# Kernel tuning notes

Measured on AMD Instinct MI355X. Metric: run time of the kernel, lower is better.

The kernel has to match this reference:

```python
import jax, jax.numpy as jnp
import numpy as np

N, D, V = 4096, 2048, 65536
IGNORE_INDEX = -100


def setup_inputs() -> dict:
    key = jax.random.key(0)
    k1, k2, k3 = jax.random.split(key, 3)
    e = jax.random.normal(k1, (N, D), dtype=jnp.float32)
    c = jax.random.normal(k2, (V, D), dtype=jnp.float32) * (D ** -0.5)
    targets = jax.random.randint(k3, (N,), 0, V, dtype=jnp.int64)
    # sprinkle some ignore_index entries to exercise masking
    targets = jnp.where(jnp.arange(N) % 97 == 0, IGNORE_INDEX, targets)
    return {"e": e, "c": c, "targets": targets}


def reference(e, c, targets):
    # logits = e @ c^T  -> [N, V] (the big intermediate CCE avoids materializing)
    logits = jnp.einsum("nd,vd->nv", e, c)
    lse = jax.nn.logsumexp(logits, axis=-1)  # [N]
    valid = targets != IGNORE_INDEX
    safe_t = jnp.where(valid, targets, 0)
    tgt_logit = jnp.take_along_axis(logits, safe_t[:, None], axis=-1)[:, 0]
    nll = jnp.where(valid, lse - tgt_logit, 0.0)
    count = jnp.maximum(jnp.sum(valid), 1)
    return jnp.sum(nll) / count.astype(nll.dtype)
```

## Files before the change

### kernel.cpp

```cpp
#include <hip/hip_runtime.h>
#include <hip/hip_bf16.h>
#include <hip/hip_fp8.h>

typedef __bf16 bf16_t;
typedef bf16_t bf16x8 __attribute__((ext_vector_type(8)));
typedef float f32x4 __attribute__((ext_vector_type(4)));
typedef float f32x16 __attribute__((ext_vector_type(16)));
typedef int   i32x4  __attribute__((ext_vector_type(4)));
typedef int   i32x8  __attribute__((ext_vector_type(8)));

#define N_ROWS 4096
#define DIM    2048
#define VOCAB  65536
#define IGN    (-100)

#define BM 128
#define BN 128
#define BK 128
#define NT (DIM / BK)
#define NUNITS (4 * NT)
#define SCALE1 0x7F7F7F7F

#define GLOAD_LDS16(gp, lp)                                                  \
  __builtin_amdgcn_global_load_lds(                                          \
      (const __attribute__((address_space(1))) void*)(gp),                   \
      (__attribute__((address_space(3))) void*)(lp), 16, 0, 0)

__global__ __launch_bounds__(256)
void cvt_fp8(const float* __restrict__ src, unsigned char* __restrict__ dst,
             long n16, float scale) {
  long i = (long)blockIdx.x * 256 + threadIdx.x;
  long stride = (long)gridDim.x * 256;
  for (; i < n16; i += stride) {
    const float4* s = reinterpret_cast<const float4*>(src) + i * 4;
    union { unsigned char b[16]; i32x4 v; } o;
#pragma unroll
    for (int q = 0; q < 4; ++q) {
      float4 a = s[q];
      o.b[q * 4 + 0] = __hip_fp8_e4m3(a.x * scale).__x;
      o.b[q * 4 + 1] = __hip_fp8_e4m3(a.y * scale).__x;
      o.b[q * 4 + 2] = __hip_fp8_e4m3(a.z * scale).__x;
      o.b[q * 4 + 3] = __hip_fp8_e4m3(a.w * scale).__x;
    }
    *reinterpret_cast<i32x4*>(dst + i * 16) = o.v;
  }
}

__global__ __launch_bounds__(256, 2)
void lce_gemm_fp8(const unsigned char* __restrict__ E8,
                  const unsigned char* __restrict__ C8,
                  float* __restrict__ sumexp) {
  extern __shared__ unsigned char lds[];
  const int tid = threadIdx.x;
  const int lane = tid & 63, wid = tid >> 6;
  const int wr = wid >> 1, wc = wid & 1;
  const int l31 = lane & 31, lh = lane >> 5;

  const int bid = blockIdx.x;
  const int wg = (bid & 7) * 2048 + (bid >> 3);
  const int brow = (wg & 31) * BM;
  const int bcol = (wg >> 5) * BN;

  const int g0 = wid * 64 + lane;
  const int g1 = 256 + g0;
  const int prel0 = g0 * 16;
  const int prel1 = g1 * 16;
  auto mkgoff = [&](int g) {
    int w = g >> 6, i = g & 63;
    return (size_t)(w * 16 + (i >> 2)) * DIM +
           (size_t)((((i & 3) ^ ((i >> 3) & 3)) << 4));
  };
  const size_t goff0 = mkgoff(g0), goff1 = mkgoff(g1);

  const unsigned char* Ebase = E8 + (size_t)brow * DIM;
  const unsigned char* Cbase = C8 + (size_t)bcol * DIM;

  auto stage = [&](int ug) {
    const unsigned char* gb = ((ug & 1) ? Cbase : Ebase) +
                              (ug >> 2) * BK + ((ug >> 1) & 1) * 64;
    unsigned char* lb = lds + (ug & 7) * 8192;
    GLOAD_LDS16(gb + goff0, lb + prel0);
    GLOAD_LDS16(gb + goff1, lb + prel1);
  };

  const int sw = (l31 >> 1) & 3;
  auto read_frag = [&](const unsigned char* U, int s) -> i32x8 {
    const unsigned char* p =
        U + s * 2048 + (l31 >> 4) * 1024 + (l31 & 15) * 64;
    i32x4 lo = *reinterpret_cast<const i32x4*>(p + (((lh * 2)     ^ sw) << 4));
    i32x4 hi = *reinterpret_cast<const i32x4*>(p + (((lh * 2 + 1) ^ sw) << 4));
    return __builtin_shufflevector(lo, hi, 0, 1, 2, 3, 4, 5, 6, 7);
  };

  f32x16 acc[2][2];
#pragma unroll
  for (int mi = 0; mi < 2; ++mi)
#pragma unroll
    for (int ni = 0; ni < 2; ++ni)
#pragma unroll
      for (int r = 0; r < 16; ++r) acc[mi][ni][r] = 0.f;

  stage(0); stage(1); stage(2); stage(3); stage(4); stage(5);
  asm volatile("s_waitcnt vmcnt(4)" ::: "memory");
  __builtin_amdgcn_s_barrier();

  i32x8 af0[2], bf0[2], af1[2], bf1[2];

  for (int T = 0; T < NT; ++T) {
    const unsigned char* base = lds + (T & 1) * 32768;
    const unsigned char* aU0 = base;
    const unsigned char* bU0 = base + 8192;
    const unsigned char* aU1 = base + 16384;
    const unsigned char* bU1 = base + 24576;

#pragma unroll
    for (int ni = 0; ni < 2; ++ni) bf0[ni] = read_frag(bU0, wc * 2 + ni);
#pragma unroll
    for (int mi = 0; mi < 2; ++mi) af0[mi] = read_frag(aU0, wr * 2 + mi);
    __builtin_amdgcn_sched_barrier(0);
#pragma unroll
    for (int ni = 0; ni < 2; ++ni) bf1[ni] = read_frag(bU1, wc * 2 + ni);
#pragma unroll
    for (int mi = 0; mi < 2; ++mi) af1[mi] = read_frag(aU1, wr * 2 + mi);
    __builtin_amdgcn_sched_barrier(0);

    stage(4 * T + 6);
    stage(4 * T + 7);
    asm volatile("s_waitcnt lgkmcnt(8)" ::: "memory");
    __builtin_amdgcn_sched_barrier(0);
    __builtin_amdgcn_s_setprio(1);
#pragma unroll
    for (int mi = 0; mi < 2; ++mi)
#pragma unroll
      for (int ni = 0; ni < 2; ++ni)
        acc[mi][ni] = __builtin_amdgcn_mfma_scale_f32_32x32x64_f8f6f4(
            af0[mi], bf0[ni], acc[mi][ni],
            0, 0, 0, SCALE1, 0, SCALE1);
    __builtin_amdgcn_s_setprio(0);
    __builtin_amdgcn_s_barrier();

    {
      const int ug = 4 * T + 8;
      if (ug < NUNITS) stage(ug);
      if (ug + 1 < NUNITS) stage(ug + 1);
    }
    asm volatile("s_waitcnt lgkmcnt(0)" ::: "memory");
    __builtin_amdgcn_sched_barrier(0);
    __builtin_amdgcn_s_setprio(1);
#pragma unroll
    for (int mi = 0; mi < 2; ++mi)
#pragma unroll
      for (int ni = 0; ni < 2; ++ni)
        acc[mi][ni] = __builtin_amdgcn_mfma_scale_f32_32x32x64_f8f6f4(
            af1[mi], bf1[ni], acc[mi][ni],
            0, 0, 0, SCALE1, 0, SCALE1);
    __builtin_amdgcn_s_setprio(0);
    if (T < NT - 1) {
      if (T < NT - 2) asm volatile("s_waitcnt vmcnt(4)" ::: "memory");
      else            asm volatile("s_waitcnt vmcnt(0)" ::: "memory");
    }
    __builtin_amdgcn_s_barrier();
  }

#pragma unroll
  for (int mi = 0; mi < 2; ++mi) {
    float p[16];
#pragma unroll
    for (int r = 0; r < 16; ++r)
      p[r] = __expf(acc[mi][0][r] * 0.125f) + __expf(acc[mi][1][r] * 0.125f);
#pragma unroll
    for (int m = 1; m < 32; m <<= 1)
#pragma unroll
      for (int r = 0; r < 16; ++r) p[r] += __shfl_xor(p[r], m, 64);
    if (l31 == 0) {
#pragma unroll
      for (int r = 0; r < 16; ++r) {
        const int row = brow + wr * 64 + mi * 32 + (r & 3) + 8 * (r >> 2) + 4 * lh;
        atomicAdd(&sumexp[row], p[r]);
      }
    }
  }
}

#define FBM 128
#define FBN 128
#define FBK 64
#define FNK (DIM / FBK)
#define FTHREADS 512

__global__ __launch_bounds__(FTHREADS, 4)
void lce_gemm_f32(const float* __restrict__ E, const float* __restrict__ C,
                  float* __restrict__ sumexp) {
  extern __shared__ unsigned char lds[];
  const int tid  = threadIdx.x;
  const int brow = blockIdx.x * FBM;
  const int bcol = blockIdx.y * FBN;

  float4 ra[4], rb[4];
  auto ld = [&](int k0) {
#pragma unroll
    for (int i = 0; i < 4; ++i) {
      int f = tid + i * FTHREADS;
      int r = f >> 4;
      int c = (f & 15) << 2;
      ra[i] = *reinterpret_cast<const float4*>(&E[(size_t)(brow + r) * DIM + k0 + c]);
      rb[i] = *reinterpret_cast<const float4*>(&C[(size_t)(bcol + r) * DIM + k0 + c]);
    }
  };
  auto st = [&](int buf) {
    unsigned char* a = lds + buf * 32768;
    unsigned char* b = a + 16384;
#pragma unroll
    for (int i = 0; i < 4; ++i) {
      int f  = tid + i * FTHREADS;
      int r  = f >> 4;
      int cbb = (f & 15) << 3;
      int off = r * 128 + (cbb ^ ((r & 7) << 4));
      union { bf16_t h[4]; unsigned long long u; } pa, pb;
      pa.h[0] = (bf16_t)ra[i].x; pa.h[1] = (bf16_t)ra[i].y;
      pa.h[2] = (bf16_t)ra[i].z; pa.h[3] = (bf16_t)ra[i].w;
      pb.h[0] = (bf16_t)rb[i].x; pb.h[1] = (bf16_t)rb[i].y;
      pb.h[2] = (bf16_t)rb[i].z; pb.h[3] = (bf16_t)rb[i].w;
      *reinterpret_cast<unsigned long long*>(a + off) = pa.u;
      *reinterpret_cast<unsigned long long*>(b + off) = pb.u;
    }
  };

  f32x4 acc[4][2];
#pragma unroll
  for (int mi = 0; mi < 4; ++mi)
#pragma unroll
    for (int ni = 0; ni < 2; ++ni) acc[mi][ni] = (f32x4){0.f, 0.f, 0.f, 0.f};

  const int lane = tid & 63, wid = tid >> 6;
  const int wr = wid >> 2, wc = wid & 3;
  const int l15 = lane & 15, lg = lane >> 4;
  const int swz = (l15 & 7) << 4;

  auto comp = [&](int buf) {
    const unsigned char* a = lds + buf * 32768;
    const unsigned char* b = a + 16384;
#pragma unroll
    for (int kk = 0; kk < 2; ++kk) {
      const int cbase = (kk * 64 + lg * 16) ^ swz;
      bf16x8 af[4], bfr[2];
#pragma unroll
      for (int mi = 0; mi < 4; ++mi)
        af[mi] = *reinterpret_cast<const bf16x8*>(
            a + (wr * 64 + mi * 16 + l15) * 128 + cbase);
#pragma unroll
      for (int ni = 0; ni < 2; ++ni)
        bfr[ni] = *reinterpret_cast<const bf16x8*>(
            b + (wc * 32 + ni * 16 + l15) * 128 + cbase);
#pragma unroll
      for (int mi = 0; mi < 4; ++mi)
#pragma unroll
        for (int ni = 0; ni < 2; ++ni)
          acc[mi][ni] = __builtin_amdgcn_mfma_f32_16x16x32_bf16(
              af[mi], bfr[ni], acc[mi][ni], 0, 0, 0);
    }
  };

  ld(0);
  st(0);
  for (int kt = 0; kt < FNK; ++kt) {
    __syncthreads();
    if (kt + 1 < FNK) ld((kt + 1) * FBK);
    comp(kt & 1);
    if (kt + 1 < FNK) st((kt + 1) & 1);
  }

#pragma unroll
  for (int mi = 0; mi < 4; ++mi) {
    float p[4];
#pragma unroll
    for (int j = 0; j < 4; ++j)
      p[j] = __expf(acc[mi][0][j]) + __expf(acc[mi][1][j]);
#pragma unroll
    for (int m = 1; m < 16; m <<= 1)
#pragma unroll
      for (int j = 0; j < 4; ++j) p[j] += __shfl_xor(p[j], m, 64);
    if (l15 == 0) {
      int row = brow + wr * 64 + mi * 16 + lg * 4;
#pragma unroll
      for (int j = 0; j < 4; ++j) atomicAdd(&sumexp[row + j], p[j]);
    }
  }
}

__global__ __launch_bounds__(256)
void lce_tgt(const float* __restrict__ E, const float* __restrict__ C,
             const int* __restrict__ T, float* __restrict__ tgt) {
  int w = (int)((blockIdx.x * blockDim.x + threadIdx.x) >> 6);
  int lane = threadIdx.x & 63;
  if (w >= N_ROWS) return;
  int t = T[w];
  float s = 0.f;
  if (t != IGN) {
    const float4* er = reinterpret_cast<const float4*>(E + (size_t)w * DIM);
    const float4* cr = reinterpret_cast<const float4*>(C + (size_t)t * DIM);
#pragma unroll
    for (int i = 0; i < DIM / 4 / 64; ++i) {
      float4 a = er[lane + i * 64];
      float4 b = cr[lane + i * 64];
      s = fmaf(a.x, b.x, s); s = fmaf(a.y, b.y, s);
      s = fmaf(a.z, b.z, s); s = fmaf(a.w, b.w, s);
    }
#pragma unroll
    for (int m = 1; m < 64; m <<= 1) s += __shfl_xor(s, m, 64);
  }
  if (lane == 0) tgt[w] = s;
}

__global__ __launch_bounds__(256)
void lce_finalize(const float* __restrict__ sumexp, const float* __restrict__ tgt,
                  const int* __restrict__ T, float* __restrict__ out) {
  int tid = threadIdx.x;
  float nll = 0.f, cnt = 0.f;
  for (int n = tid; n < N_ROWS; n += 256) {
    if (T[n] != IGN) {
      nll += logf(sumexp[n]) - tgt[n];
      cnt += 1.f;
    }
  }
#pragma unroll
  for (int m = 1; m < 64; m <<= 1) {
    nll += __shfl_xor(nll, m, 64);
    cnt += __shfl_xor(cnt, m, 64);
  }
  __shared__ float sn[4], sc[4];
  if ((tid & 63) == 0) { sn[tid >> 6] = nll; sc[tid >> 6] = cnt; }
  __syncthreads();
  if (tid == 0) {
    float a = 0.f, b = 0.f;
#pragma unroll
    for (int i = 0; i < 4; ++i) { a += sn[i]; b += sc[i]; }
    out[0] = a / fmaxf(b, 1.f);
  }
}

extern "C" void kernel_launch(void* const* d_in, const int* in_sizes, int n_in,
                              void* d_out, int out_size, void* d_ws, size_t ws_size,
                              hipStream_t stream) {
  const float* E = (const float*)d_in[0];
  const float* C = (const float*)d_in[1];
  const int*   T = (const int*)d_in[2];
  float* out = (float*)d_out;

  unsigned char* ws = (unsigned char*)d_ws;
  float* sumexp = (float*)ws;
  float* tgt    = (float*)(ws + 16384);
  unsigned char* E8 = ws + 32768;
  unsigned char* C8 = E8 + (size_t)N_ROWS * DIM;

  const size_t need = 32768 + (size_t)N_ROWS * DIM + (size_t)VOCAB * DIM;

  hipMemsetAsync(sumexp, 0, N_ROWS * sizeof(float), stream);

  if (ws_size >= need) {
    cvt_fp8<<<2048, 256, 0, stream>>>(E, E8, (long)N_ROWS * DIM / 16, 1.0f);
    cvt_fp8<<<2048, 256, 0, stream>>>(C, C8, (long)VOCAB * DIM / 16, 8.0f);
    lce_gemm_fp8<<<dim3((N_ROWS / BM) * (VOCAB / BN)), 256, 65536, stream>>>(E8, C8, sumexp);
  } else {
    lce_gemm_f32<<<dim3(N_ROWS / FBM, VOCAB / FBN), FTHREADS, 65536, stream>>>(E, C, sumexp);
  }

  lce_tgt<<<dim3((N_ROWS * 64) / 256), 256, 0, stream>>>(E, C, T, tgt);
  lce_finalize<<<dim3(1), 256, 0, stream>>>(sumexp, tgt, T, out);
}
```

Baseline: 910.3 us.

## Use 8-wave workgroups with quad-buffered LDS pipeline in FP8 GEMM

Doubles the workgroup to 512 threads (2x4 wave grid), so each wave computes a 64x32 tile with two accumulators, and each thread issues one global-to-LDS load per unit instead of two. LDS grows to 128 KB with four stages, prefetching three K-tiles ahead, and a single barrier per iteration replaces two. The aim is deeper latency hiding and lower per-wave register pressure. The cost is likely one resident workgroup per CU because of the LDS size, and less fragment reuse per MFMA.

```diff
diff --git a/kernel.cpp b/kernel.cpp
--- a/kernel.cpp
+++ b/kernel.cpp
@@ -46,14 +46,14 @@
   }
 }
 
-__global__ __launch_bounds__(256, 2)
+__global__ __launch_bounds__(512, 2)
 void lce_gemm_fp8(const unsigned char* __restrict__ E8,
                   const unsigned char* __restrict__ C8,
                   float* __restrict__ sumexp) {
   extern __shared__ unsigned char lds[];
   const int tid = threadIdx.x;
   const int lane = tid & 63, wid = tid >> 6;
-  const int wr = wid >> 1, wc = wid & 1;
+  const int wr = wid >> 2, wc = wid & 3;
   const int l31 = lane & 31, lh = lane >> 5;
 
   const int bid = blockIdx.x;
@@ -62,15 +62,13 @@
   const int bcol = (wg >> 5) * BN;
 
   const int g0 = wid * 64 + lane;
-  const int g1 = 256 + g0;
   const int prel0 = g0 * 16;
-  const int prel1 = g1 * 16;
   auto mkgoff = [&](int g) {
     int w = g >> 6, i = g & 63;
     return (size_t)(w * 16 + (i >> 2)) * DIM +
            (size_t)((((i & 3) ^ ((i >> 3) & 3)) << 4));
   };
-  const size_t goff0 = mkgoff(g0), goff1 = mkgoff(g1);
+  const size_t goff0 = mkgoff(g0);
 
   const unsigned char* Ebase = E8 + (size_t)brow * DIM;
   const unsigned char* Cbase = C8 + (size_t)bcol * DIM;
@@ -78,9 +76,8 @@
   auto stage = [&](int ug) {
     const unsigned char* gb = ((ug & 1) ? Cbase : Ebase) +
                               (ug >> 2) * BK + ((ug >> 1) & 1) * 64;
-    unsigned char* lb = lds + (ug & 7) * 8192;
+    unsigned char* lb = lds + (ug & 15) * 8192;
     GLOAD_LDS16(gb + goff0, lb + prel0);
-    GLOAD_LDS16(gb + goff1, lb + prel1);
   };
 
   const int sw = (l31 >> 1) & 3;
@@ -92,82 +89,69 @@
     return __builtin_shufflevector(lo, hi, 0, 1, 2, 3, 4, 5, 6, 7);
   };
 
-  f32x16 acc[2][2];
+  f32x16 acc[2];
 #pragma unroll
   for (int mi = 0; mi < 2; ++mi)
 #pragma unroll
-    for (int ni = 0; ni < 2; ++ni)
-#pragma unroll
-      for (int r = 0; r < 16; ++r) acc[mi][ni][r] = 0.f;
-
-  stage(0); stage(1); stage(2); stage(3); stage(4); stage(5);
-  asm volatile("s_waitcnt vmcnt(4)" ::: "memory");
-  __builtin_amdgcn_s_barrier();
-
-  i32x8 af0[2], bf0[2], af1[2], bf1[2];
+    for (int r = 0; r < 16; ++r) acc[mi][r] = 0.f;
+
+#pragma unroll
+  for (int h = 0; h < 12; ++h) stage(h);
+
+  i32x8 af0[2], af1[2], bf0, bf1;
 
   for (int T = 0; T < NT; ++T) {
-    const unsigned char* base = lds + (T & 1) * 32768;
+    if (T < NT - 2)      asm volatile("s_waitcnt vmcnt(8)" ::: "memory");
+    else if (T == NT - 2) asm volatile("s_waitcnt vmcnt(4)" ::: "memory");
+    else                  asm volatile("s_waitcnt vmcnt(0)" ::: "memory");
+    __builtin_amdgcn_s_barrier();
+
+    const unsigned char* base = lds + (T & 3) * 32768;
     const unsigned char* aU0 = base;
     const unsigned char* bU0 = base + 8192;
     const unsigned char* aU1 = base + 16384;
     const unsigned char* bU1 = base + 24576;
 
-#pragma unroll
-    for (int ni = 0; ni < 2; ++ni) bf0[ni] = read_frag(bU0, wc * 2 + ni);
+    bf0 = read_frag(bU0, wc);
 #pragma unroll
     for (int mi = 0; mi < 2; ++mi) af0[mi] = read_frag(aU0, wr * 2 + mi);
     __builtin_amdgcn_sched_barrier(0);
-#pragma unroll
-    for (int ni = 0; ni < 2; ++ni) bf1[ni] = read_frag(bU1, wc * 2 + ni);
+    bf1 = read_frag(bU1, wc);
 #pragma unroll
     for (int mi = 0; mi < 2; ++mi) af1[mi] = read_frag(aU1, wr * 2 + mi);
     __builtin_amdgcn_sched_barrier(0);
 
-    stage(4 * T + 6);
-    stage(4 * T + 7);
-    asm volatile("s_waitcnt lgkmcnt(8)" ::: "memory");
+    {
+      const int ug0 = 4 * (T + 3);
+#pragma unroll
+      for (int u = 0; u < 4; ++u)
+        if (ug0 + u < NUNITS) stage(ug0 + u);
+    }
+
+    asm volatile("s_waitcnt lgkmcnt(6)" ::: "memory");
     __builtin_amdgcn_sched_barrier(0);
     __builtin_amdgcn_s_setprio(1);
 #pragma unroll
     for (int mi = 0; mi < 2; ++mi)
-#pragma unroll
-      for (int ni = 0; ni < 2; ++ni)
-        acc[mi][ni] = __builtin_amdgcn_mfma_scale_f32_32x32x64_f8f6f4(
-            af0[mi], bf0[ni], acc[mi][ni],
-            0, 0, 0, SCALE1, 0, SCALE1);
+      acc[mi] = __builtin_amdgcn_mfma_scale_f32_32x32x64_f8f6f4(
+          af0[mi], bf0, acc[mi], 0, 0, 0, SCALE1, 0, SCALE1);
     __builtin_amdgcn_s_setprio(0);
-    __builtin_amdgcn_s_barrier();
-
-    {
-      const int ug = 4 * T + 8;
-      if (ug < NUNITS) stage(ug);
-      if (ug + 1 < NUNITS) stage(ug + 1);
-    }
+
     asm volatile("s_waitcnt lgkmcnt(0)" ::: "memory");
     __builtin_amdgcn_sched_barrier(0);
     __builtin_amdgcn_s_setprio(1);
 #pragma unroll
     for (int mi = 0; mi < 2; ++mi)
-#pragma unroll
-      for (int ni = 0; ni < 2; ++ni)
-        acc[mi][ni] = __builtin_amdgcn_mfma_scale_f32_32x32x64_f8f6f4(
-            af1[mi], bf1[ni], acc[mi][ni],
-            0, 0, 0, SCALE1, 0, SCALE1);
+      acc[mi] = __builtin_amdgcn_mfma_scale_f32_32x32x64_f8f6f4(
+          af1[mi], bf1, acc[mi], 0, 0, 0, SCALE1, 0, SCALE1);
     __builtin_amdgcn_s_setprio(0);
-    if (T < NT - 1) {
-      if (T < NT - 2) asm volatile("s_waitcnt vmcnt(4)" ::: "memory");
-      else            asm volatile("s_waitcnt vmcnt(0)" ::: "memory");
-    }
-    __builtin_amdgcn_s_barrier();
   }
 
 #pragma unroll
   for (int mi = 0; mi < 2; ++mi) {
     float p[16];
 #pragma unroll
-    for (int r = 0; r < 16; ++r)
-      p[r] = __expf(acc[mi][0][r] * 0.125f) + __expf(acc[mi][1][r] * 0.125f);
+    for (int r = 0; r < 16; ++r) p[r] = __expf(acc[mi][r] * 0.125f);
 #pragma unroll
     for (int m = 1; m < 32; m <<= 1)
 #pragma unroll
@@ -360,7 +344,7 @@
   if (ws_size >= need) {
     cvt_fp8<<<2048, 256, 0, stream>>>(E, E8, (long)N_ROWS * DIM / 16, 1.0f);
     cvt_fp8<<<2048, 256, 0, stream>>>(C, C8, (long)VOCAB * DIM / 16, 8.0f);
-    lce_gemm_fp8<<<dim3((N_ROWS / BM) * (VOCAB / BN)), 256, 65536, stream>>>(E8, C8, sumexp);
+    lce_gemm_fp8<<<dim3((N_ROWS / BM) * (VOCAB / BN)), 512, 131072, stream>>>(E8, C8, sumexp);
   } else {
     lce_gemm_f32<<<dim3(N_ROWS / FBM, VOCAB / FBN), FTHREADS, 65536, stream>>>(E, C, sumexp);
   }
```

Result: slower. 1.243 ms (+36.5%).
